# Performance work log

Measured on AMD Instinct MI355X. Metric: run time of the kernel, lower is better.

## Reference

```python
import jax, jax.numpy as jnp
import numpy as np

EPS = 1e-7

def setup_inputs() -> dict:
    key = jax.random.key(0)
    k1, k2, k3, k4 = jax.random.split(key, 4)
    B, F, NA = 4096, 512, 8192
    return {
        "x_real": jax.random.normal(k1, (B, F), dtype=jnp.float32),
        "x_imag": jax.random.normal(k2, (B, F), dtype=jnp.float32),
        "att_real": jax.random.normal(k3, (NA, F), dtype=jnp.float32),
        "att_imag": jax.random.normal(k4, (NA, F), dtype=jnp.float32),
        "alpha": jnp.float32(0.2),
        "top_k": 32,
    }

def _l2_normalize(v):
    # faiss.normalize_L2: divide each row by its L2 norm
    return v / jnp.linalg.norm(v, axis=1, keepdims=True)

def reference(x_real, x_imag, att_real, att_imag, alpha, top_k):
    # Database = queries themselves + attention tokens (complex, kept as re/im)
    db_re = jnp.concatenate([x_real, att_real], axis=0)   # [N, F]
    db_im = jnp.concatenate([x_imag, att_imag], axis=0)   # [N, F]
    db_reim = _l2_normalize(jnp.concatenate([db_re, db_im], axis=1))  # [N, 2F]
    q_reim = _l2_normalize(jnp.concatenate([x_real, x_imag], axis=1)) # [B, 2F]
    # IndexFlatIP on L2-normalized vectors = cosine similarity brute-force search
    sims = jnp.einsum('bd,nd->bn', q_reim, db_reim)        # [B, N]
    k = min(top_k, db_reim.shape[0])
    _, nn_idx = jax.lax.top_k(sims, k)                     # [B, K]
    nb_re = db_re[nn_idx]                                  # [B, K, F]
    nb_im = db_im[nn_idx]                                  # [B, K, F]
    # circular (polar) mean aggregation
    rho = jnp.sqrt(nb_re * nb_re + nb_im * nb_im) + EPS    # |z| + eps
    phi = jnp.arctan2(nb_im, nb_re)                        # angle(z)
    mean_rho = rho.mean(axis=1)                            # [B, F]
    mean_phi = jnp.arctan2(jnp.sin(phi).mean(axis=1), jnp.cos(phi).mean(axis=1))
    agg_re = mean_rho * jnp.cos(mean_phi)
    agg_im = mean_rho * jnp.sin(mean_phi)
    a = jnp.clip(alpha, 0.0, 1.0)
    out_re = (1.0 - a) * x_real + a * agg_re
    out_im = (1.0 - a) * x_imag + a * agg_im
    return jnp.stack([out_re, out_im], axis=0)             # [2, B, F]
```

## Files before the change

kernel.cpp:

```cpp
#include <hip/hip_runtime.h>
#include <math.h>

#define BQ   4096
#define FD   512
#define NATT 8192
#define NDB  (BQ + NATT)
#define DD   (2 * FD)
#define KTOP 32
#define EPSF 1e-7f
#define DEL2 0.004f

#define QT   32
#define NT   96
#define NTILES (2048 + 528)

typedef __attribute__((ext_vector_type(8))) short bf16x8;
typedef __attribute__((ext_vector_type(8))) unsigned short u16x8;
typedef __attribute__((ext_vector_type(4))) float f32x4;

__device__ unsigned short g_pk[(size_t)NDB * DD];
__device__ float g_sims[(size_t)BQ * NDB];
__device__ float g_tmax[(size_t)BQ * NT];
__device__ float g_ninv[NDB];

__device__ __forceinline__ unsigned fkey(unsigned u) {
    return u ^ (unsigned)(((int)u >> 31) | 0x80000000);
}
__device__ __forceinline__ float unfkey(unsigned fk) {
    unsigned u = (fk & 0x80000000u) ? (fk ^ 0x80000000u) : ~fk;
    return __uint_as_float(u);
}
__device__ __forceinline__ unsigned short f2bf(float f) {
    unsigned u = __float_as_uint(f);
    return (unsigned short)((u + 0x7FFFu + ((u >> 16) & 1u)) >> 16);
}
__device__ __forceinline__ float frsq(float x) {
#if __has_builtin(__builtin_amdgcn_rsqf)
    return __builtin_amdgcn_rsqf(x);
#else
    return rsqrtf(x);
#endif
}
__device__ __forceinline__ void gld16(const void* g, void* l) {
    __builtin_amdgcn_global_load_lds(
        (const __attribute__((address_space(1))) void*)g,
        (__attribute__((address_space(3))) void*)l, 16, 0, 0);
}

__global__ __launch_bounds__(256) void normalize_kernel(
        const float* __restrict__ x_real, const float* __restrict__ x_imag,
        const float* __restrict__ att_real, const float* __restrict__ att_imag) {
    int t = threadIdx.x;
    int r = t >> 4;
    int l16 = t & 15;
    int row = blockIdx.x * 16 + r;
    const float *re, *im;
    if (row < BQ) { re = x_real + (size_t)row * FD;          im = x_imag + (size_t)row * FD; }
    else          { re = att_real + (size_t)(row - BQ) * FD; im = att_imag + (size_t)(row - BQ) * FD; }

    float4 vre[8], vim[8];
    float ss = 0.0f;
#pragma unroll
    for (int i = 0; i < 8; ++i) {
        vre[i] = *(const float4*)(re + l16 * 32 + i * 4);
        vim[i] = *(const float4*)(im + l16 * 32 + i * 4);
        ss += vre[i].x * vre[i].x + vre[i].y * vre[i].y + vre[i].z * vre[i].z + vre[i].w * vre[i].w;
        ss += vim[i].x * vim[i].x + vim[i].y * vim[i].y + vim[i].z * vim[i].z + vim[i].w * vim[i].w;
    }
#pragma unroll
    for (int o = 1; o < 16; o <<= 1) ss += __shfl_xor(ss, o);
    float ninv = frsq(ss);
    if (l16 == 0) g_ninv[row] = ninv;

    auto emit = [&](const float4* v, int kchunk) {
        unsigned short hi[32];
#pragma unroll
        for (int i = 0; i < 8; ++i) {
            float vals[4] = {v[i].x, v[i].y, v[i].z, v[i].w};
#pragma unroll
            for (int j = 0; j < 4; ++j) hi[i * 4 + j] = f2bf(vals[j] * ninv);
        }
        size_t cb = ((size_t)((row >> 7) * 32 + kchunk)) * 4096 + (size_t)(row & 127) * 8;
#pragma unroll
        for (int kc = 0; kc < 4; ++kc)
            *(u16x8*)(g_pk + cb + kc * 1024) = *(u16x8*)&hi[kc * 8];
    };
    emit(vre, l16);
    emit(vim, 16 + l16);
}

__global__ __launch_bounds__(256) void gemm_mfma() {
    __shared__ unsigned short smem[2 * 4096];
    const int t = threadIdx.x;
    const int lane = t & 63, wid = t >> 6;
    const int wr = wid >> 1, wc = wid & 1;
    const int kc = lane >> 4, fr = lane & 15;

    int tid = blockIdx.x;
    int bm, bn; bool mirror = false;
    if (tid < 2048) { bm = tid >> 6; bn = QT + (tid & 63); }
    else {
        int t2 = tid - 2048;
        int r = 0, off = 0;
        while (t2 >= off + (QT - r)) { off += QT - r; ++r; }
        bm = r; bn = r + (t2 - off);
        mirror = (bn != bm);
    }

    f32x4 acc[4][4];
#pragma unroll
    for (int m = 0; m < 4; ++m)
#pragma unroll
        for (int n = 0; n < 4; ++n) acc[m][n] = (f32x4){0.f, 0.f, 0.f, 0.f};

    for (int c = 0; c < 32; ++c) {
        const unsigned short* apk = g_pk + ((size_t)(bm * 32 + c)) * 4096;
        const unsigned short* bpk = g_pk + ((size_t)(bn * 32 + c)) * 4096;
#pragma unroll
        for (int i = 0; i < 2; ++i) {
            int s = t + i * 256;
            gld16(apk + (size_t)s * 8, &smem[s * 8]);
            gld16(bpk + (size_t)s * 8, &smem[4096 + s * 8]);
        }
        __syncthreads();

        bf16x8 ah[4], bh[4];
#pragma unroll
        for (int m = 0; m < 4; ++m) {
            int ra = wr * 64 + m * 16 + fr;
            ah[m] = *(const bf16x8*)&smem[(kc * 128 + ra) * 8];
            int rb = wc * 64 + m * 16 + fr;
            bh[m] = *(const bf16x8*)&smem[4096 + (kc * 128 + rb) * 8];
        }
#pragma unroll
        for (int m = 0; m < 4; ++m)
#pragma unroll
            for (int n = 0; n < 4; ++n)
                acc[m][n] = __builtin_amdgcn_mfma_f32_16x16x32_bf16(ah[m], bh[n], acc[m][n], 0, 0, 0);
        __syncthreads();
    }
    const int crow0 = bm * 128 + wr * 64 + kc * 4;
    const int ccol0 = bn * 128 + wc * 64 + fr;
#pragma unroll
    for (int m = 0; m < 4; ++m)
#pragma unroll
        for (int n = 0; n < 4; ++n)
#pragma unroll
            for (int j = 0; j < 4; ++j)
                g_sims[(size_t)(crow0 + m * 16 + j) * NDB + ccol0 + n * 16] = acc[m][n][j];

    if (mirror) {
#pragma unroll
        for (int m = 0; m < 4; ++m)
#pragma unroll
            for (int n = 0; n < 4; ++n) {
                size_t r = (size_t)(bn * 128 + wc * 64 + n * 16 + fr);
                size_t cix = (size_t)(bm * 128 + wr * 64 + m * 16 + kc * 4);
                *(f32x4*)&g_sims[r * NDB + cix] = acc[m][n];
            }
    }

    float* rowhalf = (float*)smem;
    float* colhalf = (float*)smem + 256;
#pragma unroll
    for (int m = 0; m < 4; ++m)
#pragma unroll
        for (int j = 0; j < 4; ++j) {
            float v = fmaxf(fmaxf(acc[m][0][j], acc[m][1][j]),
                            fmaxf(acc[m][2][j], acc[m][3][j]));
#pragma unroll
            for (int o = 1; o < 16; o <<= 1) v = fmaxf(v, __shfl_xor(v, o));
            if (fr == 0) rowhalf[(wr * 64 + m * 16 + kc * 4 + j) * 2 + wc] = v;
        }
    if (mirror) {
#pragma unroll
        for (int n = 0; n < 4; ++n) {
            float v = acc[0][n][0];
#pragma unroll
            for (int m = 0; m < 4; ++m)
#pragma unroll
                for (int j = 0; j < 4; ++j) v = fmaxf(v, acc[m][n][j]);
            v = fmaxf(v, __shfl_xor(v, 16));
            v = fmaxf(v, __shfl_xor(v, 32));
            if (kc == 0) colhalf[(wc * 64 + n * 16 + fr) * 2 + wr] = v;
        }
    }
    __syncthreads();
    if (t < 128) {
        g_tmax[(size_t)(bm * 128 + t) * NT + bn] = fmaxf(rowhalf[t * 2], rowhalf[t * 2 + 1]);
        if (mirror)
            g_tmax[(size_t)(bn * 128 + t) * NT + bm] = fmaxf(colhalf[t * 2], colhalf[t * 2 + 1]);
    }
}

__global__ __launch_bounds__(256) void topk_agg_kernel(
        const float* __restrict__ x_real, const float* __restrict__ x_imag,
        const float* __restrict__ att_real, const float* __restrict__ att_imag,
        const float* __restrict__ alpha_p, float* __restrict__ out) {
    __shared__ float stm[96];
    __shared__ unsigned char tlist[96];
    __shared__ unsigned long long cand[1024];
    __shared__ unsigned long long skey[64];
    __shared__ unsigned long long rkey[64];
    __shared__ int ridx[64];
    __shared__ int s_idx[KTOP];
    __shared__ float qre[FD], qim[FD];
    __shared__ unsigned s_cnt;
    __shared__ int s_ntile, s_S, s_R;
    __shared__ float s_T, s_V32;
    __shared__ unsigned long long s_red[4];
    __shared__ unsigned long long s_last;
    int b = blockIdx.x, t = threadIdx.x;
    int wave = t >> 6, lane = t & 63;

    if (t < 96) stm[t] = g_tmax[(size_t)b * NT + t];
    if (t < 128) *(float4*)&qre[t * 4] = *(const float4*)(x_real + (size_t)b * FD + t * 4);
    else         *(float4*)&qim[(t - 128) * 4] = *(const float4*)(x_imag + (size_t)b * FD + (t - 128) * 4);
    if (t == 0) { s_cnt = 0; s_ntile = 0; s_S = 0; s_R = 0; }
    __syncthreads();

    if (t < 96) {
        float v = stm[t];
        int cnt = 0;
        for (int i = 0; i < 96; ++i) {
            float o = stm[i];
            cnt += (o > v) || (o == v && i < t);
        }
        if (cnt == KTOP - 1) s_T = v;
    }
    __syncthreads();
    const float Tm = s_T - DEL2;

    if (t < 96 && stm[t] >= Tm) { int p = atomicAdd(&s_ntile, 1); tlist[p] = (unsigned char)t; }
    __syncthreads();
    const int ntile = s_ntile;

    const float* rowp = g_sims + (size_t)b * NDB;
    for (int base = 0; base < ntile; base += 8) {
        int ti = base + (t >> 5);
        if (ti < ntile) {
            int tile = tlist[ti];
            int c4 = (t & 31) * 4;
            float4 v = *(const float4*)(rowp + tile * 128 + c4);
            int gidx = tile * 128 + c4;
            if (v.x >= Tm) { unsigned p = atomicAdd(&s_cnt, 1u); if (p < 1024) cand[p] = ((unsigned long long)fkey(__float_as_uint(v.x)) << 32) | (unsigned)(~(gidx + 0)); }
            if (v.y >= Tm) { unsigned p = atomicAdd(&s_cnt, 1u); if (p < 1024) cand[p] = ((unsigned long long)fkey(__float_as_uint(v.y)) << 32) | (unsigned)(~(gidx + 1)); }
            if (v.z >= Tm) { unsigned p = atomicAdd(&s_cnt, 1u); if (p < 1024) cand[p] = ((unsigned long long)fkey(__float_as_uint(v.z)) << 32) | (unsigned)(~(gidx + 2)); }
            if (v.w >= Tm) { unsigned p = atomicAdd(&s_cnt, 1u); if (p < 1024) cand[p] = ((unsigned long long)fkey(__float_as_uint(v.w)) << 32) | (unsigned)(~(gidx + 3)); }
        }
    }
    __syncthreads();
    unsigned cnt_raw = s_cnt;
    int c = (int)cnt_raw; if (c > 1024) c = 1024;

    if (c <= 64) {
        if (wave == 0) {
            unsigned long long vv = (lane < c) ? cand[lane] : 0ull;
#pragma unroll
            for (int k = 2; k <= 64; k <<= 1)
#pragma unroll
                for (int j = k >> 1; j > 0; j >>= 1) {
                    unsigned long long o = __shfl_xor(vv, j);
                    bool lower = (lane & j) == 0;
                    bool desc  = (lane & k) == 0;
                    bool keepmax = (lower == desc);
                    vv = keepmax ? (vv > o ? vv : o) : (vv < o ? vv : o);
                }
            skey[lane] = vv;
        }
        __syncthreads();
    } else {
        unsigned long long last = ~0ull;
        for (int it = 0; it < 64; ++it) {
            unsigned long long m = 0;
            for (int i = t; i < c; i += 256) { unsigned long long k = cand[i]; if (k < last && k > m) m = k; }
#pragma unroll
            for (int o = 32; o > 0; o >>= 1) { unsigned long long x = __shfl_xor(m, o); m = x > m ? x : m; }
            if (lane == 0) s_red[wave] = m;
            __syncthreads();
            if (t == 0) {
                unsigned long long w = s_red[0];
#pragma unroll
                for (int i = 1; i < 4; ++i) w = s_red[i] > w ? s_red[i] : w;
                skey[it] = w; s_last = w;
            }
            __syncthreads();
            last = s_last;
        }
    }
    if (t == 0) s_V32 = unfkey((unsigned)(skey[31] >> 32));
    __syncthreads();
    const float V32 = s_V32;
    bool fallback = (cnt_raw > 1024);
    if (c > 64) {
        float v63 = unfkey((unsigned)(skey[63] >> 32));
        fallback = fallback || (v63 >= V32 - DEL2);
    }
    const float qninv = g_ninv[b];

    if (!fallback) {
        if (wave == 0) {
            unsigned long long k = skey[lane];
            float v = (k != 0) ? unfkey((unsigned)(k >> 32)) : -INFINITY;
            int idx = (int)(~(unsigned)k);
            bool sure = v > V32 + DEL2;
            bool amb  = !sure && v >= V32 - DEL2;
            unsigned long long smask = __ballot(sure);
            int S = __popcll(smask);
            if (sure) s_idx[lane] = idx;
            if (amb)  ridx[lane - S] = idx;
            if (lane == 0) { s_S = S; }
            unsigned long long amask = __ballot(amb);
            if (lane == 0) { s_R = __popcll(amask); }
        }
        __syncthreads();
        int S = s_S, R = s_R;
        for (int r = wave; r < R; r += 4) {
            int j = ridx[r];
            const float *dre, *dim_;
            if (j < BQ) { dre = x_real + (size_t)j * FD; dim_ = x_imag + (size_t)j * FD; }
            else        { dre = att_real + (size_t)(j - BQ) * FD; dim_ = att_imag + (size_t)(j - BQ) * FD; }
            float4 a0 = *(const float4*)&qre[lane * 8], a1 = *(const float4*)&qre[lane * 8 + 4];
            float4 b0 = *(const float4*)(dre + lane * 8), b1 = *(const float4*)(dre + lane * 8 + 4);
            float4 c0 = *(const float4*)&qim[lane * 8], c1 = *(const float4*)&qim[lane * 8 + 4];
            float4 d0 = *(const float4*)(dim_ + lane * 8), d1 = *(const float4*)(dim_ + lane * 8 + 4);
            float s = a0.x * b0.x + a0.y * b0.y + a0.z * b0.z + a0.w * b0.w
                    + a1.x * b1.x + a1.y * b1.y + a1.z * b1.z + a1.w * b1.w
                    + c0.x * d0.x + c0.y * d0.y + c0.z * d0.z + c0.w * d0.w
                    + c1.x * d1.x + c1.y * d1.y + c1.z * d1.z + c1.w * d1.w;
#pragma unroll
            for (int o = 32; o > 0; o >>= 1) s += __shfl_xor(s, o);
            float v = s * qninv * g_ninv[j];
            if (lane == 0) rkey[r] = ((unsigned long long)fkey(__float_as_uint(v)) << 32) | (unsigned)(~j);
        }
        __syncthreads();
        if (wave == 0) {
            unsigned long long vv = (lane < R) ? rkey[lane] : 0ull;
#pragma unroll
            for (int k = 2; k <= 64; k <<= 1)
#pragma unroll
                for (int j = k >> 1; j > 0; j >>= 1) {
                    unsigned long long o = __shfl_xor(vv, j);
                    bool lower = (lane & j) == 0;
                    bool desc  = (lane & k) == 0;
                    bool keepmax = (lower == desc);
                    vv = keepmax ? (vv > o ? vv : o) : (vv < o ? vv : o);
                }
            if (lane < KTOP - S) s_idx[S + lane] = (int)(~(unsigned)vv);
        }
        __syncthreads();
    } else {
        for (int r = wave; r < c; r += 4) {
            int j = (int)(~(unsigned)cand[r]);
            const float *dre, *dim_;
            if (j < BQ) { dre = x_real + (size_t)j * FD; dim_ = x_imag + (size_t)j * FD; }
            else        { dre = att_real + (size_t)(j - BQ) * FD; dim_ = att_imag + (size_t)(j - BQ) * FD; }
            float4 a0 = *(const float4*)&qre[lane * 8], a1 = *(const float4*)&qre[lane * 8 + 4];
            float4 b0 = *(const float4*)(dre + lane * 8), b1 = *(const float4*)(dre + lane * 8 + 4);
            float4 c0 = *(const float4*)&qim[lane * 8], c1 = *(const float4*)&qim[lane * 8 + 4];
            float4 d0 = *(const float4*)(dim_ + lane * 8), d1 = *(const float4*)(dim_ + lane * 8 + 4);
            float s = a0.x * b0.x + a0.y * b0.y + a0.z * b0.z + a0.w * b0.w
                    + a1.x * b1.x + a1.y * b1.y + a1.z * b1.z + a1.w * b1.w
                    + c0.x * d0.x + c0.y * d0.y + c0.z * d0.z + c0.w * d0.w
                    + c1.x * d1.x + c1.y * d1.y + c1.z * d1.z + c1.w * d1.w;
#pragma unroll
            for (int o = 32; o > 0; o >>= 1) s += __shfl_xor(s, o);
            float v = s * qninv * g_ninv[j];
            if (lane == 0) cand[r] = ((unsigned long long)fkey(__float_as_uint(v)) << 32) | (unsigned)(~j);
        }
        __syncthreads();
        unsigned long long last = ~0ull;
        for (int it = 0; it < KTOP; ++it) {
            unsigned long long m = 0;
            for (int i = t; i < c; i += 256) { unsigned long long k = cand[i]; if (k < last && k > m) m = k; }
#pragma unroll
            for (int o = 32; o > 0; o >>= 1) { unsigned long long x = __shfl_xor(m, o); m = x > m ? x : m; }
            if (lane == 0) s_red[wave] = m;
            __syncthreads();
            if (t == 0) {
                unsigned long long w = s_red[0];
#pragma unroll
                for (int i = 1; i < 4; ++i) w = s_red[i] > w ? s_red[i] : w;
                s_idx[it] = (int)(~(unsigned)w); s_last = w;
            }
            __syncthreads();
            last = s_last;
        }
    }
    __syncthreads();

    float a = alpha_p[0];
    a = fminf(fmaxf(a, 0.0f), 1.0f);
    int f = 2 * t;
    float sr0 = 0, sc0 = 0, ss0 = 0, sr1 = 0, sc1 = 0, ss1 = 0;
    for (int k = 0; k < KTOP; ++k) {
        int idx = s_idx[k];
        const float *re, *im;
        if (idx < BQ) { re = x_real + (size_t)idx * FD;          im = x_imag + (size_t)idx * FD; }
        else          { re = att_real + (size_t)(idx - BQ) * FD; im = att_imag + (size_t)(idx - BQ) * FD; }
        float2 vr = *(const float2*)(re + f);
        float2 vi = *(const float2*)(im + f);
        float s0 = vr.x * vr.x + vi.x * vi.x;
        if (s0 > 0.0f) {
            float iv = frsq(s0);
            sr0 += s0 * iv; sc0 += vr.x * iv; ss0 += vi.x * iv;
        } else sc0 += 1.0f;
        float s1 = vr.y * vr.y + vi.y * vi.y;
        if (s1 > 0.0f) {
            float iv = frsq(s1);
            sr1 += s1 * iv; sc1 += vr.y * iv; ss1 += vi.y * iv;
        } else sc1 += 1.0f;
    }
    const float inv = 1.0f / KTOP;
    float mr0 = sr0 * inv + EPSF, mc0 = sc0 * inv, ms0 = ss0 * inv;
    float mr1 = sr1 * inv + EPSF, mc1 = sc1 * inv, ms1 = ss1 * inv;
    float q0 = mc0 * mc0 + ms0 * ms0;
    float q1 = mc1 * mc1 + ms1 * ms1;
    float i0 = (q0 > 0.0f) ? frsq(q0) : 0.0f;
    float i1 = (q1 > 0.0f) ? frsq(q1) : 0.0f;
    float c0v = (q0 > 0.0f) ? mc0 * i0 : 1.0f;
    float s0v = ms0 * i0;
    float c1v = (q1 > 0.0f) ? mc1 * i1 : 1.0f;
    float s1v = ms1 * i1;
    size_t obase = (size_t)b * FD + f;
    float2 xr = *(const float2*)(x_real + obase);
    float2 xi = *(const float2*)(x_imag + obase);
    float2 outr = make_float2((1.0f - a) * xr.x + a * (mr0 * c0v),
                              (1.0f - a) * xr.y + a * (mr1 * c1v));
    float2 outi = make_float2((1.0f - a) * xi.x + a * (mr0 * s0v),
                              (1.0f - a) * xi.y + a * (mr1 * s1v));
    *(float2*)(out + obase) = outr;
    *(float2*)(out + (size_t)BQ * FD + obase) = outi;
}

extern "C" void kernel_launch(void* const* d_in, const int* in_sizes, int n_in,
                              void* d_out, int out_size, void* d_ws, size_t ws_size,
                              hipStream_t stream) {
    const float* x_real   = (const float*)d_in[0];
    const float* x_imag   = (const float*)d_in[1];
    const float* att_real = (const float*)d_in[2];
    const float* att_imag = (const float*)d_in[3];
    const float* alpha    = (const float*)d_in[4];
    float* out = (float*)d_out;

    normalize_kernel<<<NDB / 16, 256, 0, stream>>>(x_real, x_imag, att_real, att_imag);
    gemm_mfma<<<NTILES, 256, 0, stream>>>();
    topk_agg_kernel<<<BQ, 256, 0, stream>>>(x_real, x_imag, att_real, att_imag, alpha, out);
}
```

Before: 333.0 us.

## Split top-k selection and aggregation kernels; add two-wave bitonic merge path

Splits the fused top-k/aggregation kernel into a selection kernel that writes indices to a global buffer and a separate aggregation kernel, so each kernel's register and shared-memory footprint can allow higher occupancy. It also adds a fast path for 65-128 candidates: two waves each bitonic-sort 64 candidates, then a merge step keeps the top 64, which avoids the serial 64-iteration block-wide max-extraction loop. The costs are an extra kernel launch and a small global round trip for the indices.

```diff
diff --git a/kernel.cpp b/kernel.cpp
--- a/kernel.cpp
+++ b/kernel.cpp
@@ -22,6 +22,7 @@
 __device__ float g_sims[(size_t)BQ * NDB];
 __device__ float g_tmax[(size_t)BQ * NT];
 __device__ float g_ninv[NDB];
+__device__ int   g_topk[BQ * KTOP];
 
 __device__ __forceinline__ unsigned fkey(unsigned u) {
     return u ^ (unsigned)(((int)u >> 31) | 0x80000000);
@@ -45,6 +46,20 @@
     __builtin_amdgcn_global_load_lds(
         (const __attribute__((address_space(1))) void*)g,
         (__attribute__((address_space(3))) void*)l, 16, 0, 0);
+}
+
+__device__ __forceinline__ unsigned long long bitonic64(unsigned long long vv, int lane) {
+#pragma unroll
+    for (int k = 2; k <= 64; k <<= 1)
+#pragma unroll
+        for (int j = k >> 1; j > 0; j >>= 1) {
+            unsigned long long o = __shfl_xor(vv, j);
+            bool lower = (lane & j) == 0;
+            bool desc  = (lane & k) == 0;
+            bool keepmax = (lower == desc);
+            vv = keepmax ? (vv > o ? vv : o) : (vv < o ? vv : o);
+        }
+    return vv;
 }
 
 __global__ __launch_bounds__(256) void normalize_kernel(
@@ -193,14 +208,14 @@
     }
 }
 
-__global__ __launch_bounds__(256) void topk_agg_kernel(
+__global__ __launch_bounds__(256) void select_kernel(
         const float* __restrict__ x_real, const float* __restrict__ x_imag,
-        const float* __restrict__ att_real, const float* __restrict__ att_imag,
-        const float* __restrict__ alpha_p, float* __restrict__ out) {
+        const float* __restrict__ att_real, const float* __restrict__ att_imag) {
     __shared__ float stm[96];
     __shared__ unsigned char tlist[96];
     __shared__ unsigned long long cand[1024];
     __shared__ unsigned long long skey[64];
+    __shared__ unsigned long long skey2[64];
     __shared__ unsigned long long rkey[64];
     __shared__ int ridx[64];
     __shared__ int s_idx[KTOP];
@@ -254,18 +269,24 @@
     int c = (int)cnt_raw; if (c > 1024) c = 1024;
 
     if (c <= 64) {
+        if (wave == 0) skey[lane] = bitonic64((lane < c) ? cand[lane] : 0ull, lane);
+        __syncthreads();
+    } else if (c <= 128) {
+        if (wave < 2) {
+            int i = wave * 64 + lane;
+            unsigned long long vv = bitonic64((i < c) ? cand[i] : 0ull, lane);
+            if (wave == 0) skey[lane] = vv; else skey2[lane] = vv;
+        }
+        __syncthreads();
         if (wave == 0) {
-            unsigned long long vv = (lane < c) ? cand[lane] : 0ull;
-#pragma unroll
-            for (int k = 2; k <= 64; k <<= 1)
-#pragma unroll
-                for (int j = k >> 1; j > 0; j >>= 1) {
-                    unsigned long long o = __shfl_xor(vv, j);
-                    bool lower = (lane & j) == 0;
-                    bool desc  = (lane & k) == 0;
-                    bool keepmax = (lower == desc);
-                    vv = keepmax ? (vv > o ? vv : o) : (vv < o ? vv : o);
-                }
+            unsigned long long a = skey[lane], b2 = skey2[63 - lane];
+            unsigned long long vv = a > b2 ? a : b2;
+#pragma unroll
+            for (int j = 32; j > 0; j >>= 1) {
+                unsigned long long o = __shfl_xor(vv, j);
+                bool keepmax = (lane & j) == 0;
+                vv = keepmax ? (vv > o ? vv : o) : (vv < o ? vv : o);
+            }
             skey[lane] = vv;
         }
         __syncthreads();
@@ -309,9 +330,9 @@
             int S = __popcll(smask);
             if (sure) s_idx[lane] = idx;
             if (amb)  ridx[lane - S] = idx;
-            if (lane == 0) { s_S = S; }
+            if (lane == 0) s_S = S;
             unsigned long long amask = __ballot(amb);
-            if (lane == 0) { s_R = __popcll(amask); }
+            if (lane == 0) s_R = __popcll(amask);
         }
         __syncthreads();
         int S = s_S, R = s_R;
@@ -335,17 +356,7 @@
         }
         __syncthreads();
         if (wave == 0) {
-            unsigned long long vv = (lane < R) ? rkey[lane] : 0ull;
-#pragma unroll
-            for (int k = 2; k <= 64; k <<= 1)
-#pragma unroll
-                for (int j = k >> 1; j > 0; j >>= 1) {
-                    unsigned long long o = __shfl_xor(vv, j);
-                    bool lower = (lane & j) == 0;
-                    bool desc  = (lane & k) == 0;
-                    bool keepmax = (lower == desc);
-                    vv = keepmax ? (vv > o ? vv : o) : (vv < o ? vv : o);
-                }
+            unsigned long long vv = bitonic64((lane < s_R) ? rkey[lane] : 0ull, lane);
             if (lane < KTOP - S) s_idx[S + lane] = (int)(~(unsigned)vv);
         }
         __syncthreads();
@@ -388,13 +399,23 @@
         }
     }
     __syncthreads();
-
+    if (t < KTOP) g_topk[b * KTOP + t] = s_idx[t];
+}
+
+__global__ __launch_bounds__(256) void agg_kernel(
+        const float* __restrict__ x_real, const float* __restrict__ x_imag,
+        const float* __restrict__ att_real, const float* __restrict__ att_imag,
+        const float* __restrict__ alpha_p, float* __restrict__ out) {
+    __shared__ int idxs[KTOP];
+    int b = blockIdx.x, t = threadIdx.x;
+    if (t < KTOP) idxs[t] = g_topk[b * KTOP + t];
+    __syncthreads();
     float a = alpha_p[0];
     a = fminf(fmaxf(a, 0.0f), 1.0f);
     int f = 2 * t;
     float sr0 = 0, sc0 = 0, ss0 = 0, sr1 = 0, sc1 = 0, ss1 = 0;
     for (int k = 0; k < KTOP; ++k) {
-        int idx = s_idx[k];
+        int idx = idxs[k];
         const float *re, *im;
         if (idx < BQ) { re = x_real + (size_t)idx * FD;          im = x_imag + (size_t)idx * FD; }
         else          { re = att_real + (size_t)(idx - BQ) * FD; im = att_imag + (size_t)(idx - BQ) * FD; }
@@ -445,5 +466,6 @@
 
     normalize_kernel<<<NDB / 16, 256, 0, stream>>>(x_real, x_imag, att_real, att_imag);
     gemm_mfma<<<NTILES, 256, 0, stream>>>();
-    topk_agg_kernel<<<BQ, 256, 0, stream>>>(x_real, x_imag, att_real, att_imag, alpha, out);
-}
+    select_kernel<<<BQ, 256, 0, stream>>>(x_real, x_imag, att_real, att_imag);
+    agg_kernel<<<BQ, 256, 0, stream>>>(x_real, x_imag, att_real, att_imag, alpha, out);
+}
```

After: 319.1 us. -4.2%, faster.
